# Kernel optimization log

Hardware: AMD Instinct MI355X
Metric: run time of the kernel (lower is better)

## Reference

```python
import jax, jax.numpy as jnp
import numpy as np

D = 256      # d_model
A = 64       # attn_dim
K = 16       # k_neighbors
N = 20000    # embedding table rows
B = 32768    # batch of perturbed genes
SCALE = A ** -0.5
EPS = 1e-5


def setup_inputs() -> dict:
    key = jax.random.key(0)
    ks = jax.random.split(key, 12)
    all_embs = jax.random.normal(ks[0], (N, D), dtype=jnp.float32)
    center_idx = jax.random.randint(ks[1], (B,), 0, N)
    nb_idx = jax.random.randint(ks[2], (B, K), 0, N)
    nb_weights = jax.random.uniform(ks[3], (B, K), dtype=jnp.float32)
    # learned params (torch Linear weight layout: [out, in])
    s = lambda fan_in: 1.0 / np.sqrt(fan_in)
    Wq = jax.random.uniform(ks[4], (A, D), minval=-s(D), maxval=s(D))
    Wk = jax.random.uniform(ks[5], (A, D), minval=-s(D), maxval=s(D))
    Wg = jax.random.uniform(ks[6], (D, D), minval=-s(D), maxval=s(D))
    bg = jax.random.uniform(ks[7], (D,), minval=-s(D), maxval=s(D))
    Wo = jax.random.uniform(ks[8], (D, 2 * D), minval=-s(2 * D), maxval=s(2 * D))
    bo = jax.random.uniform(ks[9], (D,), minval=-s(2 * D), maxval=s(2 * D))
    gamma = jnp.ones((D,), jnp.float32)
    beta = jnp.zeros((D,), jnp.float32)
    return dict(all_embs=all_embs, center_idx=center_idx, nb_idx=nb_idx,
                nb_weights=nb_weights, Wq=Wq, Wk=Wk, Wg=Wg, bg=bg,
                Wo=Wo, bo=bo, gamma=gamma, beta=beta)


def reference(all_embs, center_idx, nb_idx, nb_weights, Wq, Wk, Wg, bg, Wo, bo, gamma, beta):
    center = all_embs[center_idx]                      # [B, D]
    nbs = all_embs[nb_idx]                             # [B, K, D]
    q = center @ Wq.T                                  # [B, A]
    k = jnp.einsum('bkd,ad->bka', nbs, Wk)             # [B, K, A]
    logits = jnp.einsum('ba,bka->bk', q, k) * SCALE
    logits = logits + jnp.log(jnp.clip(nb_weights, 1e-6))
    attn = jax.nn.softmax(logits, axis=-1)             # [B, K]
    gate = jax.nn.sigmoid(center @ Wg.T + bg)          # [B, D]
    context = gate * jnp.einsum('bk,bkd->bd', attn, nbs)
    combined = jnp.concatenate([center, context], axis=-1)  # [B, 2D]
    enriched = combined @ Wo.T + bo                    # [B, D]
    x = enriched + center
    mu = jnp.mean(x, axis=-1, keepdims=True)
    var = jnp.var(x, axis=-1, keepdims=True)
    return (x - mu) * jax.lax.rsqrt(var + EPS) * gamma + beta
```

## Files before the change

kernel.cpp:

```cpp
#include <hip/hip_runtime.h>

#define DD 256
#define MM 16

typedef __attribute__((ext_vector_type(8))) short bfrag;
typedef __attribute__((ext_vector_type(4))) float ffrag;

__device__ __forceinline__ float lo2f(unsigned int p){ union{unsigned int i; float f;} v; v.i = p<<16; return v.f; }
__device__ __forceinline__ float hi2f(unsigned int p){ union{unsigned int i; float f;} v; v.i = p & 0xffff0000u; return v.f; }
__device__ __forceinline__ float bf2f(unsigned short u){ union{unsigned int i; float f;} v; v.i = ((unsigned int)u)<<16; return v.f; }
__device__ __forceinline__ unsigned short f2b(float x){
    union{float f; unsigned int i;} v; v.f = x;
    unsigned int r = v.i + 0x7fffu + ((v.i>>16)&1u);
    return (unsigned short)(r>>16);
}
__device__ __forceinline__ unsigned int pack2(float a, float b){
    return (unsigned int)f2b(a) | ((unsigned int)f2b(b)<<16);
}

__device__ __forceinline__ int swz256(int d, int e){
    return ((d>>4)*8 + (e>>5))*512 + (((e>>3)&3)*16 + (d&15))*8 + (e&7);
}
__device__ __forceinline__ int swz512(int d, int e){
    return ((d>>4)*16 + (e>>5))*512 + (((e>>3)&3)*16 + (d&15))*8 + (e&7);
}

extern "C" __global__ __launch_bounds__(256)
void prep_all(const float* __restrict__ Wq, const float* __restrict__ Wk,
              const float* __restrict__ Wg, const float* __restrict__ Wo,
              const float* __restrict__ embs, unsigned short* __restrict__ ws, int n8)
{
    int bid = blockIdx.x, e = threadIdx.x;
    if (bid < 256) {
        int d = bid; float acc = 0.f;
        #pragma unroll 8
        for (int a = 0; a < 64; ++a) acc = fmaf(Wq[a*256 + e], Wk[a*256 + d], acc);
        ws[swz256(d, e)] = f2b(acc);
    } else if (bid < 512) {
        int r = bid - 256;
        ws[65536 + swz256(r, e)] = f2b(Wg[r*256 + e]);
    } else if (bid < 768) {
        int r = bid - 512;
        ws[131072 + swz512(r, e)]       = f2b(Wo[r*512 + e]);
        ws[131072 + swz512(r, e + 256)] = f2b(Wo[r*512 + 256 + e]);
    } else {
        int i = (bid - 768)*256 + e;
        if (i < n8) {
            const float4* s = (const float4*)embs + (size_t)i*2;
            float4 a = s[0], b = s[1];
            uint4 o;
            o.x = pack2(a.x,a.y); o.y = pack2(a.z,a.w);
            o.z = pack2(b.x,b.y); o.w = pack2(b.z,b.w);
            ((uint4*)(ws + 262144))[i] = o;
        }
    }
}

template<bool TBF>
__device__ __forceinline__ void gather8(uint4* buf, const unsigned short* tbl,
                                        const float* embs, int idx, int p)
{
    if (TBF) {
        const unsigned short* base = tbl + (size_t)idx*DD + p*8;
        #pragma unroll
        for (int i = 0; i < 8; ++i) buf[i] = *(const uint4*)(base + i*32);
    } else {
        const float* base = embs + (size_t)idx*DD + p*8;
        #pragma unroll
        for (int i = 0; i < 8; ++i) {
            float4 a = *(const float4*)(base + i*32);
            float4 b = *(const float4*)(base + i*32 + 4);
            buf[i].x = pack2(a.x,a.y); buf[i].y = pack2(a.z,a.w);
            buf[i].z = pack2(b.x,b.y); buf[i].w = pack2(b.z,b.w);
        }
    }
}

template<bool TBF>
__global__ __launch_bounds__(256, 2)
void na_mfma3(const float* __restrict__ embs,
              const int* __restrict__ cidx,
              const int* __restrict__ nidx,
              const float* __restrict__ nbw,
              const unsigned short* __restrict__ tbl,
              const unsigned short* __restrict__ wMt,
              const unsigned short* __restrict__ wWg,
              const unsigned short* __restrict__ wWo,
              const float* __restrict__ bg,
              const float* __restrict__ bo,
              const float* __restrict__ gamma,
              const float* __restrict__ beta,
              float* __restrict__ out)
{
    __shared__ __align__(16) unsigned short s_ac[16][264];
    __shared__ __align__(16) unsigned short s_ax[16][264];
    __shared__ __align__(16) float s_t[16][260];
    __shared__ __align__(16) unsigned short s_nb[4][16][264];
    __shared__ float s_attn[4][16];
    __shared__ int   s_cidx[16];

    const int tid  = threadIdx.x;
    const int row0 = blockIdx.x * MM;
    const int lane = tid & 63, wv = tid >> 6;
    const int l15  = lane & 15, quad = lane >> 4;
    const ffrag fz = {0.f, 0.f, 0.f, 0.f};

    if (tid < 16) s_cidx[tid] = cidx[row0 + tid];
    {
        int m = tid >> 4, cs = tid & 15;
        int idx = cidx[row0 + m];
        const float4* src = (const float4*)(embs + (size_t)idx * DD + cs * 16);
        float4 a = src[0], b = src[1], c2 = src[2], d2 = src[3];
        uint4 o0, o1;
        o0.x = pack2(a.x,a.y);   o0.y = pack2(a.z,a.w);
        o0.z = pack2(b.x,b.y);   o0.w = pack2(b.z,b.w);
        o1.x = pack2(c2.x,c2.y); o1.y = pack2(c2.z,c2.w);
        o1.z = pack2(d2.x,d2.y); o1.w = pack2(d2.z,d2.w);
        uint4* dst = (uint4*)&s_ac[m][cs * 16];
        dst[0] = o0; dst[1] = o1;
    }
    __syncthreads();

    {
        ffrag at[4] = {fz,fz,fz,fz}, ag[4] = {fz,fz,fz,fz};
        const unsigned short* ar  = &s_ac[l15][quad * 8];
        const unsigned short* btA = wMt + (size_t)(wv*4)*4096 + lane*8;
        const unsigned short* bgA = wWg + (size_t)(wv*4)*4096 + lane*8;
        #pragma unroll
        for (int kc = 0; kc < 8; ++kc) {
            bfrag af = *(const bfrag*)(ar + kc*32);
            #pragma unroll
            for (int t = 0; t < 4; ++t) {
                at[t] = __builtin_amdgcn_mfma_f32_16x16x32_bf16(af, *(const bfrag*)(btA + t*4096 + kc*512), at[t], 0,0,0);
                ag[t] = __builtin_amdgcn_mfma_f32_16x16x32_bf16(af, *(const bfrag*)(bgA + t*4096 + kc*512), ag[t], 0,0,0);
            }
        }
        #pragma unroll
        for (int t = 0; t < 4; ++t) {
            int col = wv*64 + t*16 + l15;
            float bgv = bg[col];
            #pragma unroll
            for (int r = 0; r < 4; ++r) {
                int rr = quad*4 + r;
                s_t[rr][col] = at[t][r];
                float g = 1.f / (1.f + expf(-(ag[t][r] + bgv)));
                s_ax[rr][col] = f2b(g);
            }
        }
    }
    __syncthreads();

    {
        const int k = lane >> 2;
        const int p = lane & 3;
        int idxs[4];
        #pragma unroll
        for (int j = 0; j < 4; ++j)
            idxs[j] = nidx[(size_t)(row0 + 4*wv + j) * 16 + k];

        uint4 buf[2][8];
        gather8<TBF>(buf[0], tbl, embs, idxs[0], p);

        #pragma unroll
        for (int j = 0; j < 4; ++j) {
            if (j < 3) gather8<TBF>(buf[(j+1)&1], tbl, embs, idxs[j+1], p);
            const int m = 4*wv + j;
            unsigned short* nbp = &s_nb[wv][k][p*8];
            #pragma unroll
            for (int i = 0; i < 8; ++i) *(uint4*)(nbp + i*32) = buf[j&1][i];
            const float* trow = &s_t[m][p*8];
            float part = 0.f;
            #pragma unroll
            for (int i = 0; i < 8; ++i) {
                uint4 v = buf[j&1][i];
                float4 t0 = *(const float4*)(trow + i*32);
                float4 t1 = *(const float4*)(trow + i*32 + 4);
                part += lo2f(v.x)*t0.x + hi2f(v.x)*t0.y + lo2f(v.y)*t0.z + hi2f(v.y)*t0.w
                      + lo2f(v.z)*t1.x + hi2f(v.z)*t1.y + lo2f(v.w)*t1.z + hi2f(v.w)*t1.w;
            }
            part += __shfl_xor(part, 1);
            part += __shfl_xor(part, 2);
            float wgt = nbw[(size_t)(row0 + m) * 16 + k];
            float lg = part * 0.125f + logf(fmaxf(wgt, 1e-6f));
            float mx = lg;
            mx = fmaxf(mx, __shfl_xor(mx, 4));  mx = fmaxf(mx, __shfl_xor(mx, 8));
            mx = fmaxf(mx, __shfl_xor(mx, 16)); mx = fmaxf(mx, __shfl_xor(mx, 32));
            float e = expf(lg - mx);
            float s = e;
            s += __shfl_xor(s, 4);  s += __shfl_xor(s, 8);
            s += __shfl_xor(s, 16); s += __shfl_xor(s, 32);
            float attn = e / s;
            if (p == 0) s_attn[wv][k] = attn;
            float4 aw0 = *(const float4*)&s_attn[wv][0];
            float4 aw1 = *(const float4*)&s_attn[wv][4];
            float4 aw2 = *(const float4*)&s_attn[wv][8];
            float4 aw3 = *(const float4*)&s_attn[wv][12];
            float aarr[16] = {aw0.x,aw0.y,aw0.z,aw0.w, aw1.x,aw1.y,aw1.z,aw1.w,
                              aw2.x,aw2.y,aw2.z,aw2.w, aw3.x,aw3.y,aw3.z,aw3.w};
            float c0=0.f, c1=0.f, c2=0.f, c3=0.f;
            #pragma unroll
            for (int kk = 0; kk < 16; ++kk) {
                uint2 v = *(const uint2*)&s_nb[wv][kk][lane*4];
                float a = aarr[kk];
                c0 += a * lo2f(v.x); c1 += a * hi2f(v.x);
                c2 += a * lo2f(v.y); c3 += a * hi2f(v.y);
            }
            uint2 g = *(const uint2*)&s_ax[m][lane*4];
            c0 *= lo2f(g.x); c1 *= hi2f(g.x); c2 *= lo2f(g.y); c3 *= hi2f(g.y);
            uint2 o; o.x = pack2(c0, c1); o.y = pack2(c2, c3);
            *(uint2*)&s_ax[m][lane*4] = o;
        }
    }
    __syncthreads();

    {
        ffrag acc[4] = {fz,fz,fz,fz};
        const unsigned short* arc = &s_ac[l15][quad * 8];
        const unsigned short* arx = &s_ax[l15][quad * 8];
        const unsigned short* bO  = wWo + (size_t)(wv*4)*8192 + lane*8;
        #pragma unroll
        for (int kc = 0; kc < 8; ++kc) {
            bfrag af = *(const bfrag*)(arc + kc*32);
            #pragma unroll
            for (int t = 0; t < 4; ++t)
                acc[t] = __builtin_amdgcn_mfma_f32_16x16x32_bf16(af, *(const bfrag*)(bO + t*8192 + kc*512), acc[t], 0,0,0);
        }
        #pragma unroll
        for (int kc = 8; kc < 16; ++kc) {
            bfrag af = *(const bfrag*)(arx + (kc-8)*32);
            #pragma unroll
            for (int t = 0; t < 4; ++t)
                acc[t] = __builtin_amdgcn_mfma_f32_16x16x32_bf16(af, *(const bfrag*)(bO + t*8192 + kc*512), acc[t], 0,0,0);
        }
        #pragma unroll
        for (int t = 0; t < 4; ++t) {
            int col = wv*64 + t*16 + l15;
            float bov = bo[col];
            #pragma unroll
            for (int r = 0; r < 4; ++r) {
                int rr = quad*4 + r;
                float ctr = embs[(size_t)s_cidx[rr] * DD + col];
                s_t[rr][col] = acc[t][r] + bov + ctr;
            }
        }
    }
    __syncthreads();

    {
        #pragma unroll
        for (int jj = 0; jj < 4; ++jj) {
            int m = wv * 4 + jj;
            float x0 = s_t[m][lane],       x1 = s_t[m][64 + lane];
            float x2 = s_t[m][128 + lane], x3 = s_t[m][192 + lane];
            float s  = x0 + x1 + x2 + x3;
            float ss = x0*x0 + x1*x1 + x2*x2 + x3*x3;
            #pragma unroll
            for (int off = 32; off >= 1; off >>= 1) {
                s  += __shfl_xor(s, off);
                ss += __shfl_xor(ss, off);
            }
            float mu  = s * (1.f/256.f);
            float var = ss * (1.f/256.f) - mu*mu;
            float rs  = rsqrtf(var + 1e-5f);
            size_t base = (size_t)(row0 + m) * DD;
            float xs[4] = {x0, x1, x2, x3};
            #pragma unroll
            for (int cc = 0; cc < 4; ++cc) {
                int dd = cc*64 + lane;
                out[base + dd] = (xs[cc] - mu) * rs * gamma[dd] + beta[dd];
            }
        }
    }
}

#define SD 260
#define KT 16
#define WS 17
extern "C" __global__ __launch_bounds__(256)
void na_f32_kernel(const float* __restrict__ embs, const int* __restrict__ center_idx,
                   const int* __restrict__ nb_idx, const float* __restrict__ nb_w,
                   const float* __restrict__ Wq, const float* __restrict__ Wk,
                   const float* __restrict__ Wg, const float* __restrict__ bg,
                   const float* __restrict__ Wo, const float* __restrict__ bo,
                   const float* __restrict__ gamma, const float* __restrict__ beta,
                   float* __restrict__ out)
{
    __shared__ __align__(16) float s_center[MM][SD];
    __shared__ __align__(16) float s_tc[MM][SD];
    __shared__ __align__(16) float s_nb[16][SD];
    __shared__ __align__(16) float s_w[DD][WS];
    __shared__ __align__(16) float s_q[MM][64];
    __shared__ float s_red[16][16];
    __shared__ float s_attn[16];
    const int tid = threadIdx.x;
    const int row0 = blockIdx.x * MM;
    const int td = tid & 63, tm = tid >> 6;
    {
        int m = tid >> 4, c = tid & 15;
        int idx = center_idx[row0 + m];
        const float4* src = (const float4*)(embs + (size_t)idx * DD) + c * 4;
        float4* dst = (float4*)&s_center[m][c * 16];
        dst[0]=src[0]; dst[1]=src[1]; dst[2]=src[2]; dst[3]=src[3];
    }
    __syncthreads();
    {
        const int a = tid & 63, mg = tid >> 6;
        float qacc[4] = {0,0,0,0};
        for (int kt = 0; kt < DD; kt += KT) {
            __syncthreads();
            { int r = tid >> 2, c4 = (tid & 3) * 4;
              *(float4*)&s_w[r][c4] = *(const float4*)(Wq + r * DD + kt + c4); }
            __syncthreads();
            #pragma unroll
            for (int kk = 0; kk < KT; kk += 4) {
                float4 b = *(const float4*)&s_w[a][kk];
                #pragma unroll
                for (int i = 0; i < 4; ++i) {
                    float4 av = *(const float4*)&s_center[4*mg + i][kt + kk];
                    qacc[i] += av.x*b.x + av.y*b.y + av.z*b.z + av.w*b.w;
                }
            }
        }
        __syncthreads();
        #pragma unroll
        for (int i = 0; i < 4; ++i) s_q[4*mg + i][a] = qacc[i];
    }
    __syncthreads();
    {
        float tacc[4][4];
        #pragma unroll
        for (int i=0;i<4;++i) { tacc[i][0]=tacc[i][1]=tacc[i][2]=tacc[i][3]=0.f; }
        for (int kk = 0; kk < 64; kk += 4) {
            float4 bk[4];
            #pragma unroll
            for (int t4 = 0; t4 < 4; ++t4)
                bk[t4] = *(const float4*)(Wk + (size_t)(kk + t4) * DD + 4 * td);
            #pragma unroll
            for (int i = 0; i < 4; ++i) {
                float4 av = *(const float4*)&s_q[4*tm + i][kk];
                tacc[i][0] += av.x*bk[0].x + av.y*bk[1].x + av.z*bk[2].x + av.w*bk[3].x;
                tacc[i][1] += av.x*bk[0].y + av.y*bk[1].y + av.z*bk[2].y + av.w*bk[3].y;
                tacc[i][2] += av.x*bk[0].z + av.y*bk[1].z + av.z*bk[2].z + av.w*bk[3].z;
                tacc[i][3] += av.x*bk[0].w + av.y*bk[1].w + av.z*bk[2].w + av.w*bk[3].w;
            }
        }
        #pragma unroll
        for (int i = 0; i < 4; ++i)
            *(float4*)&s_tc[4*tm + i][4*td] = make_float4(tacc[i][0],tacc[i][1],tacc[i][2],tacc[i][3]);
    }
    __syncthreads();
    for (int m = 0; m < MM; ++m) {
        { int k = tid >> 4, c = tid & 15;
          int idx = nb_idx[(row0 + m) * 16 + k];
          const float4* src = (const float4*)(embs + (size_t)idx * DD) + c * 4;
          float4* dst = (float4*)&s_nb[k][c * 16];
          dst[0]=src[0]; dst[1]=src[1]; dst[2]=src[2]; dst[3]=src[3]; }
        __syncthreads();
        { int k = tid >> 4, i = tid & 15;
          float acc = 0.f;
          #pragma unroll
          for (int j4 = 0; j4 < 4; ++j4) {
              float4 nv = *(const float4*)&s_nb[k][i*16 + 4*j4];
              float4 tv = *(const float4*)&s_tc[m][i*16 + 4*j4];
              acc += nv.x*tv.x + nv.y*tv.y + nv.z*tv.z + nv.w*tv.w;
          }
          s_red[k][i] = acc; }
        __syncthreads();
        if (tid < 16) {
            float lg = 0.f;
            #pragma unroll
            for (int i = 0; i < 16; ++i) lg += s_red[tid][i];
            float wv2 = nb_w[(row0 + m) * 16 + tid];
            lg = lg * 0.125f + logf(fmaxf(wv2, 1e-6f));
            float mx = lg;
            #pragma unroll
            for (int off = 8; off >= 1; off >>= 1) mx = fmaxf(mx, __shfl_xor(mx, off));
            float e = expf(lg - mx);
            float s = e;
            #pragma unroll
            for (int off = 8; off >= 1; off >>= 1) s += __shfl_xor(s, off);
            s_attn[tid] = e / s;
        }
        __syncthreads();
        { float acc = 0.f;
          #pragma unroll
          for (int k = 0; k < 16; ++k) acc += s_attn[k] * s_nb[k][tid];
          s_tc[m][tid] = acc; }
        __syncthreads();
    }
    {
        float acc[4][4];
        #pragma unroll
        for (int i=0;i<4;++i){acc[i][0]=acc[i][1]=acc[i][2]=acc[i][3]=0.f;}
        for (int kt = 0; kt < DD; kt += KT) {
            __syncthreads();
            #pragma unroll
            for (int j = 0; j < 4; ++j) {
                int r = (tid >> 2) + 64 * j, c4 = (tid & 3) * 4;
                *(float4*)&s_w[r][c4] = *(const float4*)(Wg + (size_t)r * DD + kt + c4);
            }
            __syncthreads();
            #pragma unroll
            for (int kk = 0; kk < KT; kk += 4) {
                float4 b[4];
                #pragma unroll
                for (int j = 0; j < 4; ++j) b[j] = *(const float4*)&s_w[4*td + j][kk];
                #pragma unroll
                for (int i = 0; i < 4; ++i) {
                    float4 av = *(const float4*)&s_center[4*tm + i][kt + kk];
                    #pragma unroll
                    for (int j = 0; j < 4; ++j)
                        acc[i][j] += av.x*b[j].x + av.y*b[j].y + av.z*b[j].z + av.w*b[j].w;
                }
            }
        }
        float bgv[4];
        #pragma unroll
        for (int j = 0; j < 4; ++j) bgv[j] = bg[4*td + j];
        __syncthreads();
        #pragma unroll
        for (int i = 0; i < 4; ++i)
            #pragma unroll
            for (int j = 0; j < 4; ++j) {
                float g = 1.f / (1.f + expf(-(acc[i][j] + bgv[j])));
                s_tc[4*tm + i][4*td + j] *= g;
            }
    }
    {
        float acc[4][4];
        #pragma unroll
        for (int i=0;i<4;++i){acc[i][0]=acc[i][1]=acc[i][2]=acc[i][3]=0.f;}
        for (int kt = 0; kt < 2*DD; kt += KT) {
            __syncthreads();
            #pragma unroll
            for (int j = 0; j < 4; ++j) {
                int r = (tid >> 2) + 64 * j, c4 = (tid & 3) * 4;
                *(float4*)&s_w[r][c4] = *(const float4*)(Wo + (size_t)r * 2 * DD + kt + c4);
            }
            __syncthreads();
            const float* Abase = (kt < DD) ? &s_center[0][0] : &s_tc[0][0];
            const int kb = (kt < DD) ? kt : kt - DD;
            #pragma unroll
            for (int kk = 0; kk < KT; kk += 4) {
                float4 b[4];
                #pragma unroll
                for (int j = 0; j < 4; ++j) b[j] = *(const float4*)&s_w[4*td + j][kk];
                #pragma unroll
                for (int i = 0; i < 4; ++i) {
                    float4 av = *(const float4*)(Abase + (4*tm + i) * SD + kb + kk);
                    #pragma unroll
                    for (int j = 0; j < 4; ++j)
                        acc[i][j] += av.x*b[j].x + av.y*b[j].y + av.z*b[j].z + av.w*b[j].w;
                }
            }
        }
        float bov[4];
        #pragma unroll
        for (int j = 0; j < 4; ++j) bov[j] = bo[4*td + j];
        __syncthreads();
        #pragma unroll
        for (int i = 0; i < 4; ++i)
            #pragma unroll
            for (int j = 0; j < 4; ++j)
                s_tc[4*tm + i][4*td + j] = acc[i][j] + bov[j] + s_center[4*tm + i][4*td + j];
    }
    __syncthreads();
    {
        int wv2 = tid >> 6, lane = tid & 63;
        #pragma unroll
        for (int jj = 0; jj < 4; ++jj) {
            int m = wv2 * 4 + jj;
            float x0 = s_tc[m][lane],       x1 = s_tc[m][64 + lane];
            float x2 = s_tc[m][128 + lane], x3 = s_tc[m][192 + lane];
            float s  = x0+x1+x2+x3;
            float ss = x0*x0 + x1*x1 + x2*x2 + x3*x3;
            #pragma unroll
            for (int off = 32; off >= 1; off >>= 1) { s += __shfl_xor(s, off); ss += __shfl_xor(ss, off); }
            float mu = s * (1.f/256.f);
            float var = ss * (1.f/256.f) - mu*mu;
            float rs = rsqrtf(var + 1e-5f);
            size_t base = (size_t)(row0 + m) * DD;
            float xs[4] = {x0,x1,x2,x3};
            #pragma unroll
            for (int c = 0; c < 4; ++c) {
                int dd = c*64 + lane;
                out[base + dd] = (xs[c] - mu) * rs * gamma[dd] + beta[dd];
            }
        }
    }
}

extern "C" void kernel_launch(void* const* d_in, const int* in_sizes, int n_in,
                              void* d_out, int out_size, void* d_ws, size_t ws_size,
                              hipStream_t stream) {
    const float* embs  = (const float*)d_in[0];
    const int*   cidx  = (const int*)d_in[1];
    const int*   nidx  = (const int*)d_in[2];
    const float* nbw   = (const float*)d_in[3];
    const float* Wq    = (const float*)d_in[4];
    const float* Wk    = (const float*)d_in[5];
    const float* Wg    = (const float*)d_in[6];
    const float* bg    = (const float*)d_in[7];
    const float* Wo    = (const float*)d_in[8];
    const float* bo    = (const float*)d_in[9];
    const float* gamma = (const float*)d_in[10];
    const float* beta  = (const float*)d_in[11];
    float* out = (float*)d_out;

    const int B = in_sizes[1];
    const int nemb = in_sizes[0];
    const size_t need_w = 262144 * 2;
    const size_t need_t = need_w + (size_t)nemb * 2;

    if (ws_size < need_w) {
        hipLaunchKernelGGL(na_f32_kernel, dim3(B / MM), dim3(256), 0, stream,
                           embs, cidx, nidx, nbw, Wq, Wk, Wg, bg, Wo, bo, gamma, beta, out);
        return;
    }
    unsigned short* wsb = (unsigned short*)d_ws;
    const bool use_tbl = (ws_size >= need_t) && ((nemb & 7) == 0);
    const int n8 = use_tbl ? (nemb / 8) : 0;
    const int prep_grid = 768 + (use_tbl ? (n8 + 255) / 256 : 0);
    hipLaunchKernelGGL(prep_all, dim3(prep_grid), dim3(256), 0, stream,
                       Wq, Wk, Wg, Wo, embs, wsb, n8);

    if (use_tbl) {
        hipLaunchKernelGGL(na_mfma3<true>, dim3(B / MM), dim3(256), 0, stream,
                           embs, cidx, nidx, nbw, wsb + 262144,
                           wsb, wsb + 65536, wsb + 131072,
                           bg, bo, gamma, beta, out);
    } else {
        hipLaunchKernelGGL(na_mfma3<false>, dim3(B / MM), dim3(256), 0, stream,
                           embs, cidx, nidx, nbw, (const unsigned short*)nullptr,
                           wsb, wsb + 65536, wsb + 131072,
                           bg, bo, gamma, beta, out);
    }
}
```

Measured before the change: 191.5 us.

## Keep neighbor rows in registers per lane, dropping LDS staging for attention

Measured after the change: 296.0 us. +54.6%, slower.

```diff
diff --git a/kernel.cpp b/kernel.cpp
--- a/kernel.cpp
+++ b/kernel.cpp
@@ -57,28 +57,21 @@
 }
 
 template<bool TBF>
-__device__ __forceinline__ void gather8(uint4* buf, const unsigned short* tbl,
-                                        const float* embs, int idx, int p)
+__device__ __forceinline__ uint2 load4c(const unsigned short* tbl, const float* embs,
+                                        int idx, int c0)
 {
     if (TBF) {
-        const unsigned short* base = tbl + (size_t)idx*DD + p*8;
-        #pragma unroll
-        for (int i = 0; i < 8; ++i) buf[i] = *(const uint4*)(base + i*32);
+        return *(const uint2*)(tbl + (size_t)idx*DD + c0);
     } else {
-        const float* base = embs + (size_t)idx*DD + p*8;
-        #pragma unroll
-        for (int i = 0; i < 8; ++i) {
-            float4 a = *(const float4*)(base + i*32);
-            float4 b = *(const float4*)(base + i*32 + 4);
-            buf[i].x = pack2(a.x,a.y); buf[i].y = pack2(a.z,a.w);
-            buf[i].z = pack2(b.x,b.y); buf[i].w = pack2(b.z,b.w);
-        }
+        float4 a = *(const float4*)(embs + (size_t)idx*DD + c0);
+        uint2 r; r.x = pack2(a.x, a.y); r.y = pack2(a.z, a.w);
+        return r;
     }
 }
 
 template<bool TBF>
-__global__ __launch_bounds__(256, 2)
-void na_mfma3(const float* __restrict__ embs,
+__global__ __launch_bounds__(256, 3)
+void na_mfma5(const float* __restrict__ embs,
               const int* __restrict__ cidx,
               const int* __restrict__ nidx,
               const float* __restrict__ nbw,
@@ -95,9 +88,7 @@
     __shared__ __align__(16) unsigned short s_ac[16][264];
     __shared__ __align__(16) unsigned short s_ax[16][264];
     __shared__ __align__(16) float s_t[16][260];
-    __shared__ __align__(16) unsigned short s_nb[4][16][264];
-    __shared__ float s_attn[4][16];
-    __shared__ int   s_cidx[16];
+    __shared__ int s_cidx[16];
 
     const int tid  = threadIdx.x;
     const int row0 = blockIdx.x * MM;
@@ -151,64 +142,63 @@
     __syncthreads();
 
     {
-        const int k = lane >> 2;
-        const int p = lane & 3;
-        int idxs[4];
-        #pragma unroll
-        for (int j = 0; j < 4; ++j)
-            idxs[j] = nidx[(size_t)(row0 + 4*wv + j) * 16 + k];
-
-        uint4 buf[2][8];
-        gather8<TBF>(buf[0], tbl, embs, idxs[0], p);
-
+        const int c0 = 4 * lane;
+        uint2 nbreg[2][16];
+        {
+            const int* nrow = nidx + (size_t)(row0 + 4*wv) * 16;
+            #pragma unroll
+            for (int k = 0; k < 16; ++k)
+                nbreg[0][k] = load4c<TBF>(tbl, embs, nrow[k], c0);
+        }
         #pragma unroll
         for (int j = 0; j < 4; ++j) {
-            if (j < 3) gather8<TBF>(buf[(j+1)&1], tbl, embs, idxs[j+1], p);
             const int m = 4*wv + j;
-            unsigned short* nbp = &s_nb[wv][k][p*8];
-            #pragma unroll
-            for (int i = 0; i < 8; ++i) *(uint4*)(nbp + i*32) = buf[j&1][i];
-            const float* trow = &s_t[m][p*8];
-            float part = 0.f;
-            #pragma unroll
-            for (int i = 0; i < 8; ++i) {
-                uint4 v = buf[j&1][i];
-                float4 t0 = *(const float4*)(trow + i*32);
-                float4 t1 = *(const float4*)(trow + i*32 + 4);
-                part += lo2f(v.x)*t0.x + hi2f(v.x)*t0.y + lo2f(v.y)*t0.z + hi2f(v.y)*t0.w
-                      + lo2f(v.z)*t1.x + hi2f(v.z)*t1.y + lo2f(v.w)*t1.z + hi2f(v.w)*t1.w;
-            }
-            part += __shfl_xor(part, 1);
-            part += __shfl_xor(part, 2);
-            float wgt = nbw[(size_t)(row0 + m) * 16 + k];
-            float lg = part * 0.125f + logf(fmaxf(wgt, 1e-6f));
-            float mx = lg;
-            mx = fmaxf(mx, __shfl_xor(mx, 4));  mx = fmaxf(mx, __shfl_xor(mx, 8));
-            mx = fmaxf(mx, __shfl_xor(mx, 16)); mx = fmaxf(mx, __shfl_xor(mx, 32));
-            float e = expf(lg - mx);
-            float s = e;
-            s += __shfl_xor(s, 4);  s += __shfl_xor(s, 8);
-            s += __shfl_xor(s, 16); s += __shfl_xor(s, 32);
-            float attn = e / s;
-            if (p == 0) s_attn[wv][k] = attn;
-            float4 aw0 = *(const float4*)&s_attn[wv][0];
-            float4 aw1 = *(const float4*)&s_attn[wv][4];
-            float4 aw2 = *(const float4*)&s_attn[wv][8];
-            float4 aw3 = *(const float4*)&s_attn[wv][12];
-            float aarr[16] = {aw0.x,aw0.y,aw0.z,aw0.w, aw1.x,aw1.y,aw1.z,aw1.w,
-                              aw2.x,aw2.y,aw2.z,aw2.w, aw3.x,aw3.y,aw3.z,aw3.w};
-            float c0=0.f, c1=0.f, c2=0.f, c3=0.f;
-            #pragma unroll
-            for (int kk = 0; kk < 16; ++kk) {
-                uint2 v = *(const uint2*)&s_nb[wv][kk][lane*4];
-                float a = aarr[kk];
-                c0 += a * lo2f(v.x); c1 += a * hi2f(v.x);
-                c2 += a * lo2f(v.y); c3 += a * hi2f(v.y);
-            }
-            uint2 g = *(const uint2*)&s_ax[m][lane*4];
-            c0 *= lo2f(g.x); c1 *= hi2f(g.x); c2 *= lo2f(g.y); c3 *= hi2f(g.y);
-            uint2 o; o.x = pack2(c0, c1); o.y = pack2(c2, c3);
-            *(uint2*)&s_ax[m][lane*4] = o;
+            if (j < 3) {
+                const int* nrow = nidx + (size_t)(row0 + m + 1) * 16;
+                #pragma unroll
+                for (int k = 0; k < 16; ++k)
+                    nbreg[(j+1)&1][k] = load4c<TBF>(tbl, embs, nrow[k], c0);
+            }
+            const uint2* nb = nbreg[j&1];
+            float4 t4 = *(const float4*)&s_t[m][c0];
+            float part[16];
+            #pragma unroll
+            for (int k = 0; k < 16; ++k) {
+                uint2 v = nb[k];
+                part[k] = lo2f(v.x)*t4.x + hi2f(v.x)*t4.y
+                        + lo2f(v.y)*t4.z + hi2f(v.y)*t4.w;
+            }
+            #pragma unroll
+            for (int k = 0; k < 16; ++k) {
+                float p = part[k];
+                p += __shfl_xor(p, 1);  p += __shfl_xor(p, 2);
+                p += __shfl_xor(p, 4);  p += __shfl_xor(p, 8);
+                p += __shfl_xor(p, 16); p += __shfl_xor(p, 32);
+                part[k] = p * 0.125f;
+            }
+            float mx = part[0];
+            #pragma unroll
+            for (int k = 1; k < 16; ++k) mx = fmaxf(mx, part[k]);
+            const float* wrow = nbw + (size_t)(row0 + m) * 16;
+            float att[16]; float denom = 0.f;
+            #pragma unroll
+            for (int k = 0; k < 16; ++k) {
+                float e = fmaxf(wrow[k], 1e-6f) * __expf(part[k] - mx);
+                att[k] = e; denom += e;
+            }
+            float inv = 1.f / denom;
+            float cc0=0.f, cc1=0.f, cc2=0.f, cc3=0.f;
+            #pragma unroll
+            for (int k = 0; k < 16; ++k) {
+                uint2 v = nb[k]; float a = att[k];
+                cc0 += a * lo2f(v.x); cc1 += a * hi2f(v.x);
+                cc2 += a * lo2f(v.y); cc3 += a * hi2f(v.y);
+            }
+            uint2 g = *(const uint2*)&s_ax[m][c0];
+            cc0 *= inv * lo2f(g.x); cc1 *= inv * hi2f(g.x);
+            cc2 *= inv * lo2f(g.y); cc3 *= inv * hi2f(g.y);
+            uint2 o; o.x = pack2(cc0, cc1); o.y = pack2(cc2, cc3);
+            *(uint2*)&s_ax[m][c0] = o;
         }
     }
     __syncthreads();
@@ -525,12 +515,12 @@
                        Wq, Wk, Wg, Wo, embs, wsb, n8);
 
     if (use_tbl) {
-        hipLaunchKernelGGL(na_mfma3<true>, dim3(B / MM), dim3(256), 0, stream,
+        hipLaunchKernelGGL(na_mfma5<true>, dim3(B / MM), dim3(256), 0, stream,
                            embs, cidx, nidx, nbw, wsb + 262144,
                            wsb, wsb + 65536, wsb + 131072,
                            bg, bo, gamma, beta, out);
     } else {
-        hipLaunchKernelGGL(na_mfma3<false>, dim3(B / MM), dim3(256), 0, stream,
+        hipLaunchKernelGGL(na_mfma5<false>, dim3(B / MM), dim3(256), 0, stream,
                            embs, cidx, nidx, nbw, (const unsigned short*)nullptr,
                            wsb, wsb + 65536, wsb + 131072,
                            bg, bo, gamma, beta, out);
```

## Keep center A-fragments in registers and shrink shared memory for higher occupancy

Applied to the files above, without the earlier changes.

After: 177.1 us. -7.5%, faster.

```diff
diff --git a/kernel.cpp b/kernel.cpp
--- a/kernel.cpp
+++ b/kernel.cpp
@@ -77,8 +77,8 @@
 }
 
 template<bool TBF>
-__global__ __launch_bounds__(256, 2)
-void na_mfma3(const float* __restrict__ embs,
+__global__ __launch_bounds__(256, 3)
+void na_mfma6(const float* __restrict__ embs,
               const int* __restrict__ cidx,
               const int* __restrict__ nidx,
               const float* __restrict__ nbw,
@@ -92,12 +92,12 @@
               const float* __restrict__ beta,
               float* __restrict__ out)
 {
-    __shared__ __align__(16) unsigned short s_ac[16][264];
     __shared__ __align__(16) unsigned short s_ax[16][264];
-    __shared__ __align__(16) float s_t[16][260];
+    __shared__ __align__(16) unsigned short s_t[16][264];
     __shared__ __align__(16) unsigned short s_nb[4][16][264];
     __shared__ float s_attn[4][16];
     __shared__ int   s_cidx[16];
+    float* s_x = (float*)&s_nb[0][0][0];
 
     const int tid  = threadIdx.x;
     const int row0 = blockIdx.x * MM;
@@ -106,29 +106,32 @@
     const ffrag fz = {0.f, 0.f, 0.f, 0.f};
 
     if (tid < 16) s_cidx[tid] = cidx[row0 + tid];
-    {
-        int m = tid >> 4, cs = tid & 15;
-        int idx = cidx[row0 + m];
-        const float4* src = (const float4*)(embs + (size_t)idx * DD + cs * 16);
-        float4 a = src[0], b = src[1], c2 = src[2], d2 = src[3];
-        uint4 o0, o1;
-        o0.x = pack2(a.x,a.y);   o0.y = pack2(a.z,a.w);
-        o0.z = pack2(b.x,b.y);   o0.w = pack2(b.z,b.w);
-        o1.x = pack2(c2.x,c2.y); o1.y = pack2(c2.z,c2.w);
-        o1.z = pack2(d2.x,d2.y); o1.w = pack2(d2.z,d2.w);
-        uint4* dst = (uint4*)&s_ac[m][cs * 16];
-        dst[0] = o0; dst[1] = o1;
-    }
-    __syncthreads();
+    uint4 careg[8];
+    {
+        int aidx = cidx[row0 + l15];
+        if (TBF) {
+            const unsigned short* p = tbl + (size_t)aidx*DD + quad*8;
+            #pragma unroll
+            for (int kc = 0; kc < 8; ++kc) careg[kc] = *(const uint4*)(p + kc*32);
+        } else {
+            const float* p = embs + (size_t)aidx*DD + quad*8;
+            #pragma unroll
+            for (int kc = 0; kc < 8; ++kc) {
+                float4 a = *(const float4*)(p + kc*32);
+                float4 b = *(const float4*)(p + kc*32 + 4);
+                careg[kc].x = pack2(a.x,a.y); careg[kc].y = pack2(a.z,a.w);
+                careg[kc].z = pack2(b.x,b.y); careg[kc].w = pack2(b.z,b.w);
+            }
+        }
+    }
 
     {
         ffrag at[4] = {fz,fz,fz,fz}, ag[4] = {fz,fz,fz,fz};
-        const unsigned short* ar  = &s_ac[l15][quad * 8];
         const unsigned short* btA = wMt + (size_t)(wv*4)*4096 + lane*8;
         const unsigned short* bgA = wWg + (size_t)(wv*4)*4096 + lane*8;
         #pragma unroll
         for (int kc = 0; kc < 8; ++kc) {
-            bfrag af = *(const bfrag*)(ar + kc*32);
+            bfrag af = *(const bfrag*)&careg[kc];
             #pragma unroll
             for (int t = 0; t < 4; ++t) {
                 at[t] = __builtin_amdgcn_mfma_f32_16x16x32_bf16(af, *(const bfrag*)(btA + t*4096 + kc*512), at[t], 0,0,0);
@@ -142,7 +145,7 @@
             #pragma unroll
             for (int r = 0; r < 4; ++r) {
                 int rr = quad*4 + r;
-                s_t[rr][col] = at[t][r];
+                s_t[rr][col]  = f2b(at[t][r]);
                 float g = 1.f / (1.f + expf(-(ag[t][r] + bgv)));
                 s_ax[rr][col] = f2b(g);
             }
@@ -168,24 +171,25 @@
             unsigned short* nbp = &s_nb[wv][k][p*8];
             #pragma unroll
             for (int i = 0; i < 8; ++i) *(uint4*)(nbp + i*32) = buf[j&1][i];
-            const float* trow = &s_t[m][p*8];
+            const unsigned short* trow = &s_t[m][p*8];
             float part = 0.f;
             #pragma unroll
             for (int i = 0; i < 8; ++i) {
                 uint4 v = buf[j&1][i];
-                float4 t0 = *(const float4*)(trow + i*32);
-                float4 t1 = *(const float4*)(trow + i*32 + 4);
-                part += lo2f(v.x)*t0.x + hi2f(v.x)*t0.y + lo2f(v.y)*t0.z + hi2f(v.y)*t0.w
-                      + lo2f(v.z)*t1.x + hi2f(v.z)*t1.y + lo2f(v.w)*t1.z + hi2f(v.w)*t1.w;
+                uint4 tv = *(const uint4*)(trow + i*32);
+                part += lo2f(v.x)*lo2f(tv.x) + hi2f(v.x)*hi2f(tv.x)
+                      + lo2f(v.y)*lo2f(tv.y) + hi2f(v.y)*hi2f(tv.y)
+                      + lo2f(v.z)*lo2f(tv.z) + hi2f(v.z)*hi2f(tv.z)
+                      + lo2f(v.w)*lo2f(tv.w) + hi2f(v.w)*hi2f(tv.w);
             }
             part += __shfl_xor(part, 1);
             part += __shfl_xor(part, 2);
-            float wgt = nbw[(size_t)(row0 + m) * 16 + k];
-            float lg = part * 0.125f + logf(fmaxf(wgt, 1e-6f));
+            float lg = part * 0.125f;
             float mx = lg;
             mx = fmaxf(mx, __shfl_xor(mx, 4));  mx = fmaxf(mx, __shfl_xor(mx, 8));
             mx = fmaxf(mx, __shfl_xor(mx, 16)); mx = fmaxf(mx, __shfl_xor(mx, 32));
-            float e = expf(lg - mx);
+            float wgt = fmaxf(nbw[(size_t)(row0 + m) * 16 + k], 1e-6f);
+            float e = wgt * __expf(lg - mx);
             float s = e;
             s += __shfl_xor(s, 4);  s += __shfl_xor(s, 8);
             s += __shfl_xor(s, 16); s += __shfl_xor(s, 32);
@@ -215,12 +219,11 @@
 
     {
         ffrag acc[4] = {fz,fz,fz,fz};
-        const unsigned short* arc = &s_ac[l15][quad * 8];
         const unsigned short* arx = &s_ax[l15][quad * 8];
         const unsigned short* bO  = wWo + (size_t)(wv*4)*8192 + lane*8;
         #pragma unroll
         for (int kc = 0; kc < 8; ++kc) {
-            bfrag af = *(const bfrag*)(arc + kc*32);
+            bfrag af = *(const bfrag*)&careg[kc];
             #pragma unroll
             for (int t = 0; t < 4; ++t)
                 acc[t] = __builtin_amdgcn_mfma_f32_16x16x32_bf16(af, *(const bfrag*)(bO + t*8192 + kc*512), acc[t], 0,0,0);
@@ -240,7 +243,7 @@
             for (int r = 0; r < 4; ++r) {
                 int rr = quad*4 + r;
                 float ctr = embs[(size_t)s_cidx[rr] * DD + col];
-                s_t[rr][col] = acc[t][r] + bov + ctr;
+                s_x[rr*260 + col] = acc[t][r] + bov + ctr;
             }
         }
     }
@@ -250,8 +253,9 @@
         #pragma unroll
         for (int jj = 0; jj < 4; ++jj) {
             int m = wv * 4 + jj;
-            float x0 = s_t[m][lane],       x1 = s_t[m][64 + lane];
-            float x2 = s_t[m][128 + lane], x3 = s_t[m][192 + lane];
+            const float* xr = s_x + m*260;
+            float x0 = xr[lane],       x1 = xr[64 + lane];
+            float x2 = xr[128 + lane], x3 = xr[192 + lane];
             float s  = x0 + x1 + x2 + x3;
             float ss = x0*x0 + x1*x1 + x2*x2 + x3*x3;
             #pragma unroll
@@ -525,12 +529,12 @@
                        Wq, Wk, Wg, Wo, embs, wsb, n8);
 
     if (use_tbl) {
-        hipLaunchKernelGGL(na_mfma3<true>, dim3(B / MM), dim3(256), 0, stream,
+        hipLaunchKernelGGL(na_mfma6<true>, dim3(B / MM), dim3(256), 0, stream,
                            embs, cidx, nidx, nbw, wsb + 262144,
                            wsb, wsb + 65536, wsb + 131072,
                            bg, bo, gamma, beta, out);
     } else {
-        hipLaunchKernelGGL(na_mfma3<false>, dim3(B / MM), dim3(256), 0, stream,
+        hipLaunchKernelGGL(na_mfma6<false>, dim3(B / MM), dim3(256), 0, stream,
                            embs, cidx, nidx, nbw, (const unsigned short*)nullptr,
                            wsb, wsb + 65536, wsb + 131072,
                            bg, bo, gamma, beta, out);
```
